# Optimization experiments

Hardware: AMD Instinct MI355X
Metric: run time of the kernel (lower is better)

## Reference

```python
import jax, jax.numpy as jnp
import numpy as np

K = 8
B = 3.0
DIM = 32
HID = 32
BATCH = 65536
MIN_BW = 1e-3
MIN_BH = 1e-3
MIN_D = 1e-3


def setup_inputs() -> dict:
    key = jax.random.key(0)
    ks = jax.random.split(key, 8)
    L = DIM - 1
    x = jax.random.normal(ks[0], (BATCH, DIM), jnp.float32)
    init_param = jax.random.uniform(ks[1], (3 * K - 1,), jnp.float32, -0.5, 0.5)
    # stacked per-dim FCNN weights; layer l conditions on x[:, :l+1] -> causal zero-mask
    w1 = jax.random.normal(ks[2], (L, L, HID), jnp.float32) * 0.2
    mask = (jnp.arange(L)[None, :] <= jnp.arange(L)[:, None]).astype(jnp.float32)
    w1 = w1 * mask[:, :, None]
    b1 = jax.random.normal(ks[3], (L, HID), jnp.float32) * 0.1
    w2 = jax.random.normal(ks[4], (L, HID, HID), jnp.float32) * 0.2
    b2 = jax.random.normal(ks[5], (L, HID), jnp.float32) * 0.1
    w3 = jax.random.normal(ks[6], (L, HID, 3 * K - 1), jnp.float32) * 0.2
    b3 = jax.random.normal(ks[7], (L, 3 * K - 1), jnp.float32) * 0.1
    return {"x": x, "init_param": init_param, "w1": w1, "b1": b1,
            "w2": w2, "b2": b2, "w3": w3, "b3": b3}


def _rqs_forward(x, Wu, Hu, Du):
    # x: [dim, batch]; Wu, Hu: [dim, batch, K]; Du: [dim, batch, K-1]
    inside = (x >= -B) & (x <= B)
    xc = jnp.clip(x, -B, B)
    # bin widths
    widths = jax.nn.softmax(Wu, axis=-1)
    widths = MIN_BW + (1.0 - MIN_BW * K) * widths
    cw = jnp.cumsum(widths, axis=-1)
    cw = jnp.concatenate([jnp.zeros(cw.shape[:-1] + (1,), cw.dtype), cw], axis=-1)
    cw = 2.0 * B * cw - B
    cw = cw.at[..., 0].set(-B).at[..., -1].set(B)
    widths = cw[..., 1:] - cw[..., :-1]
    # bin heights
    heights = jax.nn.softmax(Hu, axis=-1)
    heights = MIN_BH + (1.0 - MIN_BH * K) * heights
    ch = jnp.cumsum(heights, axis=-1)
    ch = jnp.concatenate([jnp.zeros(ch.shape[:-1] + (1,), ch.dtype), ch], axis=-1)
    ch = 2.0 * B * ch - B
    ch = ch.at[..., 0].set(-B).at[..., -1].set(B)
    heights = ch[..., 1:] - ch[..., :-1]
    # knot derivatives, edges pinned so softplus(const)+min_d = 1
    const = float(np.log(np.exp(1.0 - MIN_D) - 1.0))
    pad = jnp.full(Du.shape[:-1] + (1,), const, Du.dtype)
    derivs = MIN_D + jax.nn.softplus(jnp.concatenate([pad, Du, pad], axis=-1))  # [.., K+1]
    # bin search (searchsorted on cumwidths, eps bump on last edge)
    cw_s = cw.at[..., -1].add(1e-6)
    idx = jnp.sum((xc[..., None] >= cw_s).astype(jnp.int32), axis=-1) - 1
    idx = jnp.clip(idx, 0, K - 1)
    g = lambda a: jnp.take_along_axis(a, idx[..., None], axis=-1)[..., 0]
    in_cw = g(cw)
    in_w = g(widths)
    in_ch = g(ch)
    in_h = g(heights)
    in_delta = g(heights / widths)
    d0 = g(derivs)
    d1 = g(derivs[..., 1:])
    theta = (xc - in_cw) / in_w
    tt = theta * (1.0 - theta)
    num = in_h * (in_delta * theta ** 2 + d0 * tt)
    den = in_delta + (d0 + d1 - 2.0 * in_delta) * tt
    out = in_ch + num / den
    dnum = in_delta ** 2 * (d1 * theta ** 2 + 2.0 * in_delta * tt + d0 * (1.0 - theta) ** 2)
    ld = jnp.log(dnum) - 2.0 * jnp.log(den)
    out = jnp.where(inside, out, x)  # identity tails
    ld = jnp.where(inside, ld, 0.0)
    return out, ld


def reference(x, init_param, w1, b1, w2, b2, w3, b3):
    # all per-dim conditioners at once (w1 is causally masked in setup)
    h1 = jnp.tanh(jnp.einsum('bd,ldh->lbh', x[:, :DIM - 1], w1) + b1[:, None, :])
    h2 = jnp.tanh(jnp.einsum('lbh,lhg->lbg', h1, w2) + b2[:, None, :])
    out = jnp.einsum('lbh,lho->lbo', h2, w3) + b3[:, None, :]  # [dim-1, batch, 3K-1]
    p0 = jnp.broadcast_to(init_param, (1, x.shape[0], 3 * K - 1))
    params = jnp.concatenate([p0, out], axis=0)  # [dim, batch, 3K-1]
    Wu = 2.0 * B * jax.nn.softmax(params[..., :K], axis=-1)
    Hu = 2.0 * B * jax.nn.softmax(params[..., K:2 * K], axis=-1)
    Du = jax.nn.softplus(params[..., 2 * K:])
    z_t, ld = _rqs_forward(x.T, Wu, Hu, Du)  # [dim, batch]
    return z_t.T, jnp.sum(ld, axis=0)
```

## Files before the change

kernel.cpp:

```cpp
#include <hip/hip_runtime.h>
#include <hip/hip_bf16.h>
#include <cmath>

constexpr int KN   = 8;
constexpr int NPAR = 23;
constexpr int DD   = 32;
constexpr float BND   = 3.0f;
constexpr float MINBW = 1e-3f;
constexpr float MIND  = 1e-3f;

#define TPB   256
#define ROWS  256
#define GDIMS 4
#define WST   40
#define PSTH  28
#define RECB  8192

typedef __attribute__((ext_vector_type(8))) short short8;
typedef __attribute__((ext_vector_type(4))) float float4v;
typedef __attribute__((ext_vector_type(2))) __fp16 fp16x2;
typedef __attribute__((ext_vector_type(4))) _Float16 half4v;

#define RCP(x) __builtin_amdgcn_rcpf(x)

__device__ __forceinline__ short f2bf(float f) {
    unsigned u = __float_as_uint(f);
    u += 0x7fffu + ((u >> 16) & 1u);
    return (short)(u >> 16);
}

__device__ __forceinline__ int pkbf(float a, float b) {
    union { __hip_bfloat162 v; int i; } u;
    u.v = __float22bfloat162_rn(make_float2(a, b));
    return u.i;
}

__device__ __forceinline__ int pkh(float a, float b) {
    union { fp16x2 h; int i; } u;
    u.h = __builtin_amdgcn_cvt_pkrtz(a, b);
    return u.i;
}

__device__ __forceinline__ float fast_tanh(float x) {
    float e = __expf(2.0f * x);
    return 1.0f - 2.0f * RCP(e + 1.0f);
}

__device__ __forceinline__ float softplus_fast(float v) {
    return __logf(1.0f + __expf(v));
}

__device__ __forceinline__ float rqs_apply(float xv, const float* p, float& ldout) {
    float cw[KN + 1], ch[KN + 1];
    {
        float t0[KN]; float s = 0.f;
#pragma unroll
        for (int k = 0; k < KN; ++k) { t0[k] = __expf(p[k]); s += t0[k]; }
        float inv = (2.0f * BND) * RCP(s);
        float e2[KN]; float s2 = 0.f;
#pragma unroll
        for (int k = 0; k < KN; ++k) { e2[k] = __expf(inv * t0[k]); s2 += e2[k]; }
        float fac = (1.0f - MINBW * KN) * RCP(s2);
        float c = 0.f;
        cw[0] = -BND;
#pragma unroll
        for (int k = 0; k < KN; ++k) { c += MINBW + fac * e2[k]; cw[k + 1] = 2.0f * BND * c - BND; }
        cw[KN] = BND;
    }
    {
        float t0[KN]; float s = 0.f;
#pragma unroll
        for (int k = 0; k < KN; ++k) { t0[k] = __expf(p[KN + k]); s += t0[k]; }
        float inv = (2.0f * BND) * RCP(s);
        float e2[KN]; float s2 = 0.f;
#pragma unroll
        for (int k = 0; k < KN; ++k) { e2[k] = __expf(inv * t0[k]); s2 += e2[k]; }
        float fac = (1.0f - MINBW * KN) * RCP(s2);
        float c = 0.f;
        ch[0] = -BND;
#pragma unroll
        for (int k = 0; k < KN; ++k) { c += MINBW + fac * e2[k]; ch[k + 1] = 2.0f * BND * c - BND; }
        ch[KN] = BND;
    }

    float xc = fminf(fmaxf(xv, -BND), BND);
    float in_cw = cw[0], in_w = cw[1] - cw[0];
    float in_ch = ch[0], in_h = ch[1] - ch[0];
    float dl0 = 0.0f, dl1 = p[2 * KN];
    bool e0 = true, e1 = false;
#pragma unroll
    for (int k = 1; k < KN; ++k) {
        bool c = (xc >= cw[k]);
        in_cw = c ? cw[k]            : in_cw;
        in_w  = c ? (cw[k+1]-cw[k])  : in_w;
        in_ch = c ? ch[k]            : in_ch;
        in_h  = c ? (ch[k+1]-ch[k])  : in_h;
        dl0   = c ? p[2*KN + k - 1]  : dl0;
        if (k < KN - 1) dl1 = c ? p[2*KN + k] : dl1;
        if (k == 1)      e0 = !c;
        if (k == KN - 1) e1 = c;
    }
    float d0 = e0 ? 1.0f : (MIND + softplus_fast(softplus_fast(dl0)));
    float d1 = e1 ? 1.0f : (MIND + softplus_fast(softplus_fast(dl1)));

    float rw    = RCP(in_w);
    float th    = (xc - in_cw) * rw;
    float delta = in_h * rw;
    float tt    = th * (1.0f - th);
    float th2   = th * th;
    float num   = in_h * (delta * th2 + d0 * tt);
    float den   = delta + (d0 + d1 - 2.0f * delta) * tt;
    float z     = in_ch + num * RCP(den);
    float omt   = 1.0f - th;
    float dnum  = delta * delta * (d1 * th2 + 2.0f * delta * tt + d0 * omt * omt);
    float ldv   = __logf(dnum) - 2.0f * __logf(den);

    bool inside = (xv >= -BND) && (xv <= BND);
    ldout = inside ? ldv : 0.0f;
    return inside ? z : xv;
}

__device__ __forceinline__ short8 xpose_h(float4v cA, float4v cB,
                                          int odd, int sl_a, int sl_b, bool qlow) {
    int a0 = pkbf(fast_tanh(cA[0]), fast_tanh(cA[1]));
    int a1 = pkbf(fast_tanh(cA[2]), fast_tanh(cA[3]));
    int b0 = pkbf(fast_tanh(cB[0]), fast_tanh(cB[1]));
    int b1 = pkbf(fast_tanh(cB[2]), fast_tanh(cB[3]));
    int p0 = odd ? b0 : a0, p1 = odd ? b1 : a1;
    int p2 = odd ? a0 : b0, p3 = odd ? a1 : b1;
    int g0 = __shfl(p0, sl_a, 64);
    int g1 = __shfl(p1, sl_a, 64);
    int g2 = __shfl(p2, sl_b, 64);
    int g3 = __shfl(p3, sl_b, 64);
    union { int4 i; short8 s; } u;
    u.i = qlow ? make_int4(g0, g1, g2, g3) : make_int4(g2, g3, g0, g1);
    return u.s;
}

__device__ __forceinline__ float4v f4v(float4 v) {
    float4v r; r[0] = v.x; r[1] = v.y; r[2] = v.z; r[3] = v.w; return r;
}

struct WFrag {
    short8 w1a, w1b, w2a, w2b, w3a, w3b;
    float4v bA1, bB1, bA2, bB2, bA3, bB3;
};

__device__ __forceinline__ WFrag load_wfrag(const char* __restrict__ wbuf,
                                            int l, int ln, int q) {
    const char* rec = wbuf + (size_t)l * RECB;
    const short* rw = (const short*)rec;
    const float* rb = (const float*)(rec + 7680);
    WFrag f;
    f.w1a = *(const short8*)&rw[ln * WST + q * 8];
    f.w1b = *(const short8*)&rw[(16 + ln) * WST + q * 8];
    f.w2a = *(const short8*)&rw[1280 + ln * WST + q * 8];
    f.w2b = *(const short8*)&rw[1280 + (16 + ln) * WST + q * 8];
    f.w3a = *(const short8*)&rw[2560 + ln * WST + q * 8];
    f.w3b = *(const short8*)&rw[2560 + (16 + ln) * WST + q * 8];
    f.bA1 = f4v(*(const float4*)&rb[4 * q]);
    f.bB1 = f4v(*(const float4*)&rb[16 + 4 * q]);
    f.bA2 = f4v(*(const float4*)&rb[32 + 4 * q]);
    f.bB2 = f4v(*(const float4*)&rb[48 + 4 * q]);
    f.bA3 = f4v(*(const float4*)&rb[64 + 4 * q]);
    f.bB3 = f4v(*(const float4*)&rb[80 + 4 * q]);
    return f;
}

extern "C" __global__ void __launch_bounds__(256)
k_prep(const float* __restrict__ w1, const float* __restrict__ b1,
       const float* __restrict__ w2, const float* __restrict__ b2,
       const float* __restrict__ w3, const float* __restrict__ b3,
       char* __restrict__ wbuf, float* __restrict__ ldo, int B)
{
    const int l = blockIdx.x, tid = threadIdx.x;
    if (l >= 31) {
        const int zb = l - 31;
        const int chunk = B >> 6;
        float4* dst = (float4*)(ldo + (size_t)zb * chunk);
        for (int i = tid; i < (chunk >> 2); i += 256)
            dst[i] = make_float4(0.f, 0.f, 0.f, 0.f);
        return;
    }
    short* r1 = (short*)(wbuf + (size_t)l * RECB);
    short* r2 = r1 + 1280;
    short* r3 = r2 + 1280;
    float* f1 = (float*)(wbuf + (size_t)l * RECB + 7680);
    float* f2 = f1 + 32;
    float* f3 = f2 + 32;
    const float* g1 = w1 + (size_t)l * 992;
    const float* g2 = w2 + (size_t)l * 1024;
    const float* g3 = w3 + (size_t)l * 736;
    for (int i = tid; i < 1280; i += 256) {
        int n = i / WST, k = i - WST * n;
        r1[i] = (k < 31) ? f2bf(g1[k * 32 + n]) : (short)0;
        r2[i] = (k < 32) ? f2bf(g2[k * 32 + n]) : (short)0;
        r3[i] = (n < 23 && k < 32) ? f2bf(g3[k * 23 + n]) : (short)0;
    }
    if (tid < 32) { f1[tid] = b1[(size_t)l * 32 + tid]; f2[tid] = b2[(size_t)l * 32 + tid]; }
    if (tid < 32) f3[tid] = (tid < 23) ? b3[(size_t)l * 23 + tid] : 0.0f;
}

extern "C" __global__ void __launch_bounds__(TPB, 3)
k_nsf(const float* __restrict__ x,
      const float* __restrict__ p0,
      const char* __restrict__ wbuf,
      float* __restrict__ zo, float* __restrict__ ldo, int B)
{
    __shared__ __align__(16) _Float16 sP[ROWS * PSTH];

    const int tid  = threadIdx.x;
    const int lane = tid & 63;
    const int wv   = tid >> 6;
    const int q    = lane >> 4;
    const int ln   = lane & 15;
    const int qb   = q & 1;
    const bool qlow = (q < 2);
    const int s_even = ln + 32 * qb;
    const int s_odd  = s_even + 16;
    const int sl_a = qlow ? s_even : s_odd;
    const int sl_b = qlow ? s_odd  : s_even;
    const int g    = blockIdx.y;
    const int ly0  = GDIMS * g;
    const long long rowbase = (long long)blockIdx.x * ROWS;
    const long long row = rowbase + tid;

    float xarr[GDIMS];
    {
        float4 xs = *(const float4*)(x + row * DD + ly0);
        xarr[0] = xs.x; xarr[1] = xs.y; xarr[2] = xs.z; xarr[3] = xs.w;
    }

    short8 au[4];
#pragma unroll
    for (int t = 0; t < 4; ++t) {
        const int m0 = 64 * wv + 16 * t;
        const float4* xp = (const float4*)(x + (rowbase + m0 + ln) * DD + q * 8);
        float4 uu = xp[0], vv = xp[1];
        union { int4 i; short8 s; } c;
        c.i = make_int4(pkbf(uu.x, uu.y), pkbf(uu.z, uu.w),
                        pkbf(vv.x, vv.y), pkbf(vv.z, vv.w));
        au[t] = c.s;
    }

    float zreg[GDIMS];
    float ldacc = 0.0f;

    WFrag wf = load_wfrag(wbuf, (ly0 == 0) ? 0 : ly0 - 1, ln, q);

#pragma unroll
    for (int j = 0; j < GDIMS; ++j) {
        const int ly = ly0 + j;
        if (ly == 0) {
            float pr[NPAR];
#pragma unroll
            for (int k = 0; k < NPAR; ++k) pr[k] = p0[k];
            float ld;
            zreg[0] = rqs_apply(xarr[0], pr, ld);
            ldacc += ld;
            continue;
        }

        float4v cA[4], cB[4];
#pragma unroll
        for (int t = 0; t < 4; ++t) {
            cA[t] = __builtin_amdgcn_mfma_f32_16x16x32_bf16(wf.w1a, au[t], wf.bA1, 0, 0, 0);
            cB[t] = __builtin_amdgcn_mfma_f32_16x16x32_bf16(wf.w1b, au[t], wf.bB1, 0, 0, 0);
        }
        short8 h1f[4];
#pragma unroll
        for (int t = 0; t < 4; ++t)
            h1f[t] = xpose_h(cA[t], cB[t], qb, sl_a, sl_b, qlow);
#pragma unroll
        for (int t = 0; t < 4; ++t) {
            cA[t] = __builtin_amdgcn_mfma_f32_16x16x32_bf16(wf.w2a, h1f[t], wf.bA2, 0, 0, 0);
            cB[t] = __builtin_amdgcn_mfma_f32_16x16x32_bf16(wf.w2b, h1f[t], wf.bB2, 0, 0, 0);
        }
#pragma unroll
        for (int t = 0; t < 4; ++t)
            h1f[t] = xpose_h(cA[t], cB[t], qb, sl_a, sl_b, qlow);
#pragma unroll
        for (int t = 0; t < 4; ++t) {
            cA[t] = __builtin_amdgcn_mfma_f32_16x16x32_bf16(wf.w3a, h1f[t], wf.bA3, 0, 0, 0);
            cB[t] = __builtin_amdgcn_mfma_f32_16x16x32_bf16(wf.w3b, h1f[t], wf.bB3, 0, 0, 0);
        }
#pragma unroll
        for (int t = 0; t < 4; ++t) {
            const int m0 = 64 * wv + 16 * t;
            int2 pv0 = make_int2(pkh(cA[t][0], cA[t][1]), pkh(cA[t][2], cA[t][3]));
            *(int2*)&sP[(m0 + ln) * PSTH + 4 * q] = pv0;
            if (qlow) {
                int2 pv1 = make_int2(pkh(cB[t][0], cB[t][1]), pkh(cB[t][2], cB[t][3]));
                *(int2*)&sP[(m0 + ln) * PSTH + 16 + 4 * q] = pv1;
            }
        }

        WFrag wfn;
        if (j + 1 < GDIMS) wfn = load_wfrag(wbuf, ly, ln, q);

        {
            const _Float16* pp = &sP[tid * PSTH];
            float pr[24];
#pragma unroll
            for (int u = 0; u < 6; ++u) {
                half4v hv = *(const half4v*)(pp + 4 * u);
                pr[4*u+0] = (float)hv[0];
                pr[4*u+1] = (float)hv[1];
                pr[4*u+2] = (float)hv[2];
                pr[4*u+3] = (float)hv[3];
            }
            float ld;
            zreg[j] = rqs_apply(xarr[j], pr, ld);
            ldacc += ld;
        }
        if (j + 1 < GDIMS) wf = wfn;
    }

    float4 zv = make_float4(zreg[0], zreg[1], zreg[2], zreg[3]);
    *(float4*)(zo + row * DD + ly0) = zv;
    unsafeAtomicAdd(&ldo[row], ldacc);
}

extern "C" void kernel_launch(void* const* d_in, const int* in_sizes, int n_in,
                              void* d_out, int out_size, void* d_ws, size_t ws_size,
                              hipStream_t stream) {
    const float* x  = (const float*)d_in[0];
    const float* p0 = (const float*)d_in[1];
    const float* w1 = (const float*)d_in[2];
    const float* b1 = (const float*)d_in[3];
    const float* w2 = (const float*)d_in[4];
    const float* b2 = (const float*)d_in[5];
    const float* w3 = (const float*)d_in[6];
    const float* b3 = (const float*)d_in[7];

    const int B = in_sizes[0] / DD;
    float* zo  = (float*)d_out;
    float* ldo = zo + (size_t)B * DD;
    char* wbuf = (char*)d_ws;

    hipLaunchKernelGGL(k_prep, dim3(95), dim3(256), 0, stream,
                       w1, b1, w2, b2, w3, b3, wbuf, ldo, B);
    hipLaunchKernelGGL(k_nsf, dim3(B / ROWS, DD / GDIMS), dim3(TPB), 0, stream,
                       x, p0, wbuf, zo, ldo, B);
}
```

Baseline: 143.4 us.

## Cut transcendental and reciprocal count in tanh, softmax and RQS spline math

Replaces exp/log calls with native exp2/log2 builtins and pre-scaled constants. Tanh now shares one reciprocal across four values, and each softmax pair shares one reciprocal. The double softplus collapses to log2(2+exp) and the log-derivative becomes a single log of a combined ratio. Knot positions are accumulated inline instead of stored in arrays. The goal is fewer costly transcendental and reciprocal instructions in a compute-bound kernel, at some risk to numerical accuracy from clamping, the shared reciprocals and the rewritten algebra.

```diff
diff --git a/kernel.cpp b/kernel.cpp
--- a/kernel.cpp
+++ b/kernel.cpp
@@ -23,6 +23,21 @@
 
 #define RCP(x) __builtin_amdgcn_rcpf(x)
 
+#if __has_builtin(__builtin_amdgcn_exp2f)
+#define EXP2(x) __builtin_amdgcn_exp2f(x)
+#else
+#define EXP2(x) __expf((x) * 0.6931471805599453f)
+#endif
+#if __has_builtin(__builtin_amdgcn_logf)
+#define LOG2F(x) __builtin_amdgcn_logf(x)
+#else
+#define LOG2F(x) __log2f(x)
+#endif
+#define MED3(x, lo, hi) __builtin_amdgcn_fmed3f((x), (lo), (hi))
+
+constexpr float L2E = 1.4426950408889634f;
+constexpr float LN2 = 0.6931471805599453f;
+
 __device__ __forceinline__ short f2bf(float f) {
     unsigned u = __float_as_uint(f);
     u += 0x7fffu + ((u >> 16) & 1u);
@@ -41,91 +56,116 @@
     return u.i;
 }
 
-__device__ __forceinline__ float fast_tanh(float x) {
-    float e = __expf(2.0f * x);
-    return 1.0f - 2.0f * RCP(e + 1.0f);
-}
-
-__device__ __forceinline__ float softplus_fast(float v) {
-    return __logf(1.0f + __expf(v));
+__device__ __forceinline__ float4v tanh4v(float4v c) {
+    constexpr float C2L = 2.0f * L2E;
+    float e0 = EXP2(MED3(c[0], -10.f, 10.f) * C2L);
+    float e1 = EXP2(MED3(c[1], -10.f, 10.f) * C2L);
+    float e2 = EXP2(MED3(c[2], -10.f, 10.f) * C2L);
+    float e3 = EXP2(MED3(c[3], -10.f, 10.f) * C2L);
+    float a0 = e0 + 1.f, a1 = e1 + 1.f, a2 = e2 + 1.f, a3 = e3 + 1.f;
+    float p01 = a0 * a1, p23 = a2 * a3;
+    float r   = RCP(p01 * p23);
+    float r01 = r * p23;
+    float r23 = r * p01;
+    float4v o;
+    o[0] = fmaf(-2.f, r01 * a1, 1.f);
+    o[1] = fmaf(-2.f, r01 * a0, 1.f);
+    o[2] = fmaf(-2.f, r23 * a3, 1.f);
+    o[3] = fmaf(-2.f, r23 * a2, 1.f);
+    return o;
 }
 
 __device__ __forceinline__ float rqs_apply(float xv, const float* p, float& ldout) {
-    float cw[KN + 1], ch[KN + 1];
-    {
-        float t0[KN]; float s = 0.f;
-#pragma unroll
-        for (int k = 0; k < KN; ++k) { t0[k] = __expf(p[k]); s += t0[k]; }
-        float inv = (2.0f * BND) * RCP(s);
-        float e2[KN]; float s2 = 0.f;
-#pragma unroll
-        for (int k = 0; k < KN; ++k) { e2[k] = __expf(inv * t0[k]); s2 += e2[k]; }
-        float fac = (1.0f - MINBW * KN) * RCP(s2);
-        float c = 0.f;
-        cw[0] = -BND;
-#pragma unroll
-        for (int k = 0; k < KN; ++k) { c += MINBW + fac * e2[k]; cw[k + 1] = 2.0f * BND * c - BND; }
-        cw[KN] = BND;
-    }
-    {
-        float t0[KN]; float s = 0.f;
-#pragma unroll
-        for (int k = 0; k < KN; ++k) { t0[k] = __expf(p[KN + k]); s += t0[k]; }
-        float inv = (2.0f * BND) * RCP(s);
-        float e2[KN]; float s2 = 0.f;
-#pragma unroll
-        for (int k = 0; k < KN; ++k) { e2[k] = __expf(inv * t0[k]); s2 += e2[k]; }
-        float fac = (1.0f - MINBW * KN) * RCP(s2);
-        float c = 0.f;
-        ch[0] = -BND;
-#pragma unroll
-        for (int k = 0; k < KN; ++k) { c += MINBW + fac * e2[k]; ch[k + 1] = 2.0f * BND * c - BND; }
-        ch[KN] = BND;
-    }
-
-    float xc = fminf(fmaxf(xv, -BND), BND);
-    float in_cw = cw[0], in_w = cw[1] - cw[0];
-    float in_ch = ch[0], in_h = ch[1] - ch[0];
+    constexpr float C1 = 2.0f * BND * MINBW;
+    constexpr float FC = 2.0f * BND * (1.0f - MINBW * KN);
+
+    float t0w[KN], t0h[KN];
+#pragma unroll
+    for (int k = 0; k < KN; ++k) t0w[k] = EXP2(p[k] * L2E);
+#pragma unroll
+    for (int k = 0; k < KN; ++k) t0h[k] = EXP2(p[KN + k] * L2E);
+    float sw = ((t0w[0] + t0w[1]) + (t0w[2] + t0w[3]))
+             + ((t0w[4] + t0w[5]) + (t0w[6] + t0w[7]));
+    float sh = ((t0h[0] + t0h[1]) + (t0h[2] + t0h[3]))
+             + ((t0h[4] + t0h[5]) + (t0h[6] + t0h[7]));
+    float r1   = RCP(sw * sh);
+    float invw = (2.0f * BND * L2E) * (r1 * sh);
+    float invh = (2.0f * BND * L2E) * (r1 * sw);
+    float e2w[KN], e2h[KN];
+#pragma unroll
+    for (int k = 0; k < KN; ++k) e2w[k] = EXP2(t0w[k] * invw);
+#pragma unroll
+    for (int k = 0; k < KN; ++k) e2h[k] = EXP2(t0h[k] * invh);
+    float s2w = ((e2w[0] + e2w[1]) + (e2w[2] + e2w[3]))
+              + ((e2w[4] + e2w[5]) + (e2w[6] + e2w[7]));
+    float s2h = ((e2h[0] + e2h[1]) + (e2h[2] + e2h[3]))
+              + ((e2h[4] + e2h[5]) + (e2h[6] + e2h[7]));
+    float r2   = RCP(s2w * s2h);
+    float facw = FC * (r2 * s2h);
+    float fach = FC * (r2 * s2w);
+
+    float xc = MED3(xv, -BND, BND);
+
+    float w0 = fmaf(facw, e2w[0], C1);
+    float h0 = fmaf(fach, e2h[0], C1);
+    float in_cw = -BND, in_w = w0, in_ch = -BND, in_h = h0;
     float dl0 = 0.0f, dl1 = p[2 * KN];
     bool e0 = true, e1 = false;
+    float cwk = -BND + w0;
+    float chk = -BND + h0;
 #pragma unroll
     for (int k = 1; k < KN; ++k) {
-        bool c = (xc >= cw[k]);
-        in_cw = c ? cw[k]            : in_cw;
-        in_w  = c ? (cw[k+1]-cw[k])  : in_w;
-        in_ch = c ? ch[k]            : in_ch;
-        in_h  = c ? (ch[k+1]-ch[k])  : in_h;
-        dl0   = c ? p[2*KN + k - 1]  : dl0;
-        if (k < KN - 1) dl1 = c ? p[2*KN + k] : dl1;
+        float wk = fmaf(facw, e2w[k], C1);
+        float hk = fmaf(fach, e2h[k], C1);
+        bool c = (xc >= cwk);
+        in_cw = c ? cwk : in_cw;
+        in_w  = c ? wk  : in_w;
+        in_ch = c ? chk : in_ch;
+        in_h  = c ? hk  : in_h;
+        dl0   = c ? p[2 * KN + k - 1] : dl0;
+        if (k < KN - 1) dl1 = c ? p[2 * KN + k] : dl1;
         if (k == 1)      e0 = !c;
         if (k == KN - 1) e1 = c;
-    }
-    float d0 = e0 ? 1.0f : (MIND + softplus_fast(softplus_fast(dl0)));
-    float d1 = e1 ? 1.0f : (MIND + softplus_fast(softplus_fast(dl1)));
-
-    float rw    = RCP(in_w);
-    float th    = (xc - in_cw) * rw;
-    float delta = in_h * rw;
-    float tt    = th * (1.0f - th);
-    float th2   = th * th;
-    float num   = in_h * (delta * th2 + d0 * tt);
-    float den   = delta + (d0 + d1 - 2.0f * delta) * tt;
-    float z     = in_ch + num * RCP(den);
-    float omt   = 1.0f - th;
-    float dnum  = delta * delta * (d1 * th2 + 2.0f * delta * tt + d0 * omt * omt);
-    float ldv   = __logf(dnum) - 2.0f * __logf(den);
+        cwk += wk;
+        chk += hk;
+    }
+    in_w = e1 ? (BND - in_cw) : in_w;
+    in_h = e1 ? (BND - in_ch) : in_h;
+
+    float sp0 = LOG2F(2.0f + EXP2(dl0 * L2E));
+    float sp1 = LOG2F(2.0f + EXP2(dl1 * L2E));
+    float d0 = e0 ? 1.0f : fmaf(LN2, sp0, MIND);
+    float d1 = e1 ? 1.0f : fmaf(LN2, sp1, MIND);
+
+    float u  = xc - in_cw;
+    float v  = in_w - u;
+    float s  = in_w, h = in_h;
+    float uu = u * u, vv = v * v, uv = u * v;
+    float uvs = uv * s;
+    float t   = fmaf(v, v, uu);
+    float dd  = d0 + d1;
+    float DEN = fmaf(h, t, dd * uvs);
+    float rD  = RCP(DEN);
+    float NUM = fmaf(h, uu, d0 * uvs);
+    float z   = fmaf(h * NUM, rD, in_ch);
+    float t2  = fmaf(d0, vv, d1 * uu);
+    float DN  = fmaf(h + h, uv, t2 * s);
+    float h2s = (h * h) * s;
+    float larg = ((h2s * DN) * rD) * rD;
 
     bool inside = (xv >= -BND) && (xv <= BND);
-    ldout = inside ? ldv : 0.0f;
+    ldout = inside ? LN2 * LOG2F(larg) : 0.0f;
     return inside ? z : xv;
 }
 
 __device__ __forceinline__ short8 xpose_h(float4v cA, float4v cB,
                                           int odd, int sl_a, int sl_b, bool qlow) {
-    int a0 = pkbf(fast_tanh(cA[0]), fast_tanh(cA[1]));
-    int a1 = pkbf(fast_tanh(cA[2]), fast_tanh(cA[3]));
-    int b0 = pkbf(fast_tanh(cB[0]), fast_tanh(cB[1]));
-    int b1 = pkbf(fast_tanh(cB[2]), fast_tanh(cB[3]));
+    float4v tA = tanh4v(cA);
+    float4v tB = tanh4v(cB);
+    int a0 = pkbf(tA[0], tA[1]);
+    int a1 = pkbf(tA[2], tA[3]);
+    int b0 = pkbf(tB[0], tB[1]);
+    int b1 = pkbf(tB[2], tB[3]);
     int p0 = odd ? b0 : a0, p1 = odd ? b1 : a1;
     int p2 = odd ? a0 : b0, p3 = odd ? a1 : b1;
     int g0 = __shfl(p0, sl_a, 64);
```

Measured after the change: 139.0 us. 3.0% less time.
